# Performance work log

Hardware: AMD Instinct MI355X
Metric: run time of the kernel (lower is better)

The kernel has to match this reference:

```python
import jax, jax.numpy as jnp
import numpy as np

N = 50000
E = 600000
D = 128  # embedding_dimension


def _lrelu(x):
    return jax.nn.leaky_relu(x, negative_slope=0.01)


def _rgcn(x, edge_index, edge_type, rel_w, root_w, bias):
    # FastRGCNConv, num_relations=2, aggr='mean' (PyG default).
    # Compute per-relation transforms as 2 dense GEMMs, then gather per edge.
    h = jnp.einsum('nd,rde->rne', x, rel_w)          # [2, N, D]
    src, dst = edge_index[0], edge_index[1]
    msg = h[edge_type, src]                          # [E, D] gather
    agg = jax.ops.segment_sum(msg, dst, num_segments=x.shape[0])
    deg = jax.ops.segment_sum(jnp.ones((msg.shape[0],), x.dtype), dst,
                              num_segments=x.shape[0])
    agg = agg / jnp.maximum(deg, 1.0)[:, None]       # mean over in-edges
    return agg + x @ root_w + bias


def setup_inputs() -> dict:
    key = jax.random.key(0)
    ks = jax.random.split(key, 32)
    f32 = jnp.float32
    inp = {
        'des': jax.random.normal(ks[0], (N, 768), f32),
        'tweet': jax.random.normal(ks[1], (N, 768), f32),
        'num_prop': jax.random.normal(ks[2], (N, 7), f32),
        'cat_prop': jax.random.normal(ks[3], (N, 11), f32),
        'new_feature': jax.random.normal(ks[4], (N, 1), f32),
        'edge_index': jax.random.randint(ks[5], (2, E), 0, N),
        'edge_type': jax.random.randint(ks[6], (E,), 0, 2),
    }
    def lin(k, i, o, s=0.05):
        kw, kb = jax.random.split(k)
        return (jax.random.normal(kw, (i, o), f32) * s,
                jax.random.normal(kb, (o,), f32) * s)
    pf = D // 5  # 25
    inp['W_des'], inp['b_des'] = lin(ks[7], 768, pf)
    inp['W_tweet'], inp['b_tweet'] = lin(ks[8], 768, 28)
    inp['W_num'], inp['b_num'] = lin(ks[9], 7, pf)
    inp['W_cat'], inp['b_cat'] = lin(ks[10], 11, pf)
    inp['W_new'], inp['b_new'] = lin(ks[11], 1, pf)
    inp['W_in'], inp['b_in'] = lin(ks[12], D, D)
    inp['rel_w1'] = jax.random.normal(ks[13], (2, D, D), f32) * 0.05
    inp['root_w1'] = jax.random.normal(ks[14], (D, D), f32) * 0.05
    inp['bias1'] = jax.random.normal(ks[15], (D,), f32) * 0.05
    inp['rel_w2'] = jax.random.normal(ks[16], (2, D, D), f32) * 0.05
    inp['root_w2'] = jax.random.normal(ks[17], (D, D), f32) * 0.05
    inp['bias2'] = jax.random.normal(ks[18], (D,), f32) * 0.05
    inp['W_out1'], inp['b_out1'] = lin(ks[19], D, D)
    inp['W_out2'], inp['b_out2'] = lin(ks[20], D, 2)
    return inp


def reference(des, tweet, num_prop, cat_prop, new_feature,
              W_des, b_des, W_tweet, b_tweet, W_num, b_num,
              W_cat, b_cat, W_new, b_new, W_in, b_in,
              rel_w1, root_w1, bias1, rel_w2, root_w2, bias2,
              W_out1, b_out1, W_out2, b_out2,
              edge_index, edge_type):
    d = _lrelu(des @ W_des + b_des)
    t = _lrelu(tweet @ W_tweet + b_tweet)
    n = _lrelu(num_prop @ W_num + b_num)
    c = _lrelu(cat_prop @ W_cat + b_cat)
    nf = _lrelu(new_feature @ W_new + b_new)
    x = jnp.concatenate((d, t, n, c, nf), axis=1)  # [N, 128]
    x = _lrelu(x @ W_in + b_in)
    x = _rgcn(x, edge_index, edge_type, rel_w1, root_w1, bias1)
    # dropout is identity at eval time
    x = _rgcn(x, edge_index, edge_type, rel_w2, root_w2, bias2)
    x = _lrelu(x @ W_out1 + b_out1)
    return x @ W_out2 + b_out2  # [N, 2]
```

## Files before the change

### kernel.cpp

```cpp
#include <hip/hip_runtime.h>

#define N_NODES 50000
#define N_EDGES 600000
#define NPAD    50048
#define NBLK_SCAN 196

static __device__ __forceinline__ float lrelu(float v) {
    return v > 0.f ? v : 0.01f * v;
}

template<int NCOLS>
__device__ __forceinline__ void proj_body(
    const float* __restrict__ A, const float* __restrict__ W,
    float* __restrict__ P, int row, int kq)
{
    float acc[NCOLS];
    #pragma unroll
    for (int c = 0; c < NCOLS; c++) acc[c] = 0.f;

    const float4* Ar = (const float4*)(A + (size_t)row * 768 + kq * 192);
    const float*  Wp = W + (size_t)kq * 192 * NCOLS;

    #pragma unroll 8
    for (int j = 0; j < 48; j++) {
        float4 a = Ar[j];
        const float* w = Wp + j * 4 * NCOLS;
        #pragma unroll
        for (int c = 0; c < NCOLS; c++)
            acc[c] += a.x * w[c] + a.y * w[NCOLS + c]
                    + a.z * w[2 * NCOLS + c] + a.w * w[3 * NCOLS + c];
    }
    float* o = P + ((size_t)kq * N_NODES + row) * 32;
    #pragma unroll
    for (int c = 0; c < NCOLS; c++) o[c] = acc[c];
}

__global__ __launch_bounds__(256) void proj768_v4(
    const float* __restrict__ des, const float* __restrict__ Wd,
    const float* __restrict__ tw,  const float* __restrict__ Wt,
    float* __restrict__ P)
{
    const int row = blockIdx.x * 256 + threadIdx.x;
    if (row >= N_NODES) return;
    const int kq = blockIdx.y;
    if (blockIdx.z == 0) proj_body<25>(des, Wd, P, row, kq);
    else                 proj_body<28>(tw, Wt, P + (size_t)4 * N_NODES * 32, row, kq);
}

__global__ void combine_proj4(const float* __restrict__ P,
                              const float* __restrict__ bd, const float* __restrict__ bt,
                              float* __restrict__ X0)
{
    int id = blockIdx.x * 256 + threadIdx.x;
    int n = id >> 6, c = id & 63;
    if (n >= N_NODES || c >= 53) return;
    const float* base; int cc; float b;
    if (c < 25) { base = P;                              cc = c;      b = bd[cc]; }
    else        { base = P + (size_t)4 * N_NODES * 32;   cc = c - 25; b = bt[cc]; }
    float s = base[((size_t)0 * N_NODES + n) * 32 + cc]
            + base[((size_t)1 * N_NODES + n) * 32 + cc]
            + base[((size_t)2 * N_NODES + n) * 32 + cc]
            + base[((size_t)3 * N_NODES + n) * 32 + cc];
    X0[(size_t)n * 128 + c] = lrelu(s + b);
}

__global__ void small_proj_kernel(
    const float* __restrict__ nump, const float* __restrict__ catp, const float* __restrict__ newf,
    const float* __restrict__ Wn, const float* __restrict__ bn,
    const float* __restrict__ Wc, const float* __restrict__ bc,
    const float* __restrict__ Ww, const float* __restrict__ bw,
    float* __restrict__ out)
{
    int id = blockIdx.x * 256 + threadIdx.x;
    int n = id / 75, c = id % 75;
    if (n >= N_NODES) return;
    float acc; int col;
    if (c < 25) {
        col = 53 + c; acc = bn[c];
        #pragma unroll
        for (int k = 0; k < 7; k++) acc += nump[n * 7 + k] * Wn[k * 25 + c];
    } else if (c < 50) {
        int cc = c - 25; col = 78 + cc; acc = bc[cc];
        #pragma unroll
        for (int k = 0; k < 11; k++) acc += catp[n * 11 + k] * Wc[k * 25 + cc];
    } else {
        int cc = c - 50; col = 103 + cc;
        acc = bw[cc] + newf[n] * Ww[cc];
    }
    out[(size_t)n * 128 + col] = lrelu(acc);
}

template<int KTOT, bool SPLIT, bool ACT>
__global__ __launch_bounds__(256, 4) void gemm_v2(
    const float* __restrict__ A, const float* __restrict__ A2,
    const float* __restrict__ B, const float* __restrict__ B2,
    const float* __restrict__ bias, float* __restrict__ out)
{
    __shared__ float AlT[32 * 132];
    __shared__ float Bl [32 * 132];
    const int t  = threadIdx.x;
    const int r0 = blockIdx.x * 128;
    const int tx = t & 15, ty = t >> 4;

    float acc[8][8] = {};

    for (int k0 = 0; k0 < KTOT; k0 += 32) {
        #pragma unroll
        for (int i = 0; i < 4; i++) {
            int f4i = t + i * 256;
            int row = f4i >> 3, c4 = f4i & 7;
            int k = k0 + c4 * 4;
            float4 v;
            if (!SPLIT) {
                v = *(const float4*)&A[(size_t)(r0 + row) * 128 + k];
            } else {
                if (k < 256) v = *(const float4*)&A[(size_t)(r0 + row) * 256 + k];
                else         v = *(const float4*)&A2[(size_t)(r0 + row) * 128 + (k - 256)];
            }
            AlT[(c4 * 4 + 0) * 132 + row] = v.x;
            AlT[(c4 * 4 + 1) * 132 + row] = v.y;
            AlT[(c4 * 4 + 2) * 132 + row] = v.z;
            AlT[(c4 * 4 + 3) * 132 + row] = v.w;
        }
        #pragma unroll
        for (int i = 0; i < 4; i++) {
            int f4i = t + i * 256;
            int kk = f4i >> 5, c4 = f4i & 31;
            int k = k0 + kk;
            float4 v;
            if (!SPLIT) v = *(const float4*)&B[(size_t)k * 128 + c4 * 4];
            else v = (k < 256) ? *(const float4*)&B[(size_t)k * 128 + c4 * 4]
                               : *(const float4*)&B2[(size_t)(k - 256) * 128 + c4 * 4];
            *(float4*)&Bl[kk * 132 + c4 * 4] = v;
        }
        __syncthreads();
        #pragma unroll 4
        for (int k = 0; k < 32; k++) {
            float4 a0 = *(const float4*)&AlT[k * 132 + ty * 8];
            float4 a1 = *(const float4*)&AlT[k * 132 + ty * 8 + 4];
            float4 b0 = *(const float4*)&Bl [k * 132 + tx * 8];
            float4 b1 = *(const float4*)&Bl [k * 132 + tx * 8 + 4];
            float av[8] = {a0.x, a0.y, a0.z, a0.w, a1.x, a1.y, a1.z, a1.w};
            float bv[8] = {b0.x, b0.y, b0.z, b0.w, b1.x, b1.y, b1.z, b1.w};
            #pragma unroll
            for (int i = 0; i < 8; i++)
                #pragma unroll
                for (int j = 0; j < 8; j++) acc[i][j] += av[i] * bv[j];
        }
        __syncthreads();
    }
    float4 bb0 = *(const float4*)&bias[tx * 8];
    float4 bb1 = *(const float4*)&bias[tx * 8 + 4];
    float bb[8] = {bb0.x, bb0.y, bb0.z, bb0.w, bb1.x, bb1.y, bb1.z, bb1.w};
    #pragma unroll
    for (int i = 0; i < 8; i++) {
        size_t row = (size_t)(r0 + ty * 8 + i);
        float o[8];
        #pragma unroll
        for (int j = 0; j < 8; j++) {
            o[j] = acc[i][j] + bb[j];
            if (ACT) o[j] = lrelu(o[j]);
        }
        *(float4*)&out[row * 128 + tx * 8]     = make_float4(o[0], o[1], o[2], o[3]);
        *(float4*)&out[row * 128 + tx * 8 + 4] = make_float4(o[4], o[5], o[6], o[7]);
    }
}

__global__ void count_kernel(const int* __restrict__ ei, int* __restrict__ count) {
    int e = blockIdx.x * 256 + threadIdx.x;
    if (e < N_EDGES) atomicAdd(&count[ei[N_EDGES + e]], 1);
}

__global__ void scan1_kernel(const int* __restrict__ count, int* __restrict__ partial) {
    __shared__ int sm[256];
    int b = blockIdx.x, t = threadIdx.x;
    int i = b * 256 + t;
    sm[t] = (i < N_NODES) ? count[i] : 0;
    __syncthreads();
    for (int off = 128; off > 0; off >>= 1) {
        if (t < off) sm[t] += sm[t + off];
        __syncthreads();
    }
    if (t == 0) partial[b] = sm[0];
}

__global__ void scan2_kernel(int* __restrict__ partial) {
    __shared__ int sm[256];
    int t = threadIdx.x;
    int v = (t < NBLK_SCAN) ? partial[t] : 0;
    sm[t] = v; __syncthreads();
    for (int off = 1; off < 256; off <<= 1) {
        int add = (t >= off) ? sm[t - off] : 0;
        __syncthreads();
        sm[t] += add;
        __syncthreads();
    }
    partial[t] = sm[t] - v;
}

__global__ void scan3_kernel(const int* __restrict__ count, const int* __restrict__ partial,
                             int* __restrict__ offsets) {
    __shared__ int sm[256];
    int b = blockIdx.x, t = threadIdx.x;
    int i = b * 256 + t;
    int v = (i < N_NODES) ? count[i] : 0;
    sm[t] = v; __syncthreads();
    for (int off = 1; off < 256; off <<= 1) {
        int add = (t >= off) ? sm[t - off] : 0;
        __syncthreads();
        sm[t] += add;
        __syncthreads();
    }
    if (i < N_NODES) offsets[i] = partial[b] + sm[t] - v;
}

__global__ void fill_kernel(const int* __restrict__ ei, const int* __restrict__ et,
                            const int* __restrict__ offsets, int* __restrict__ cursor,
                            int* __restrict__ elist) {
    int e = blockIdx.x * 256 + threadIdx.x;
    if (e < N_EDGES) {
        int d = ei[N_EDGES + e];
        int pos = atomicAdd(&cursor[d], 1);
        elist[offsets[d] + pos] = (int)(((unsigned)ei[e]) | (((unsigned)et[e]) << 31));
    }
}

__global__ __launch_bounds__(256) void aggregate_v3(
    const float* __restrict__ x, const int* __restrict__ offsets,
    const int* __restrict__ count, const int* __restrict__ elist,
    float* __restrict__ s)
{
    int nid  = blockIdx.x * 8 + (threadIdx.x >> 5);
    int lane = threadIdx.x & 31;
    if (nid >= N_NODES) return;
    int start = offsets[nid], dg = count[nid];
    float4 a0 = make_float4(0.f, 0.f, 0.f, 0.f);
    float4 a1 = make_float4(0.f, 0.f, 0.f, 0.f);
    int i = 0;
    for (; i + 2 <= dg; i += 2) {
        int v0 = elist[start + i];
        int v1 = elist[start + i + 1];
        float4 u = ((const float4*)&x[(size_t)(v0 & 0x7FFFFFFF) * 128])[lane];
        float4 w = ((const float4*)&x[(size_t)(v1 & 0x7FFFFFFF) * 128])[lane];
        if (v0 < 0) { a1.x += u.x; a1.y += u.y; a1.z += u.z; a1.w += u.w; }
        else        { a0.x += u.x; a0.y += u.y; a0.z += u.z; a0.w += u.w; }
        if (v1 < 0) { a1.x += w.x; a1.y += w.y; a1.z += w.z; a1.w += w.w; }
        else        { a0.x += w.x; a0.y += w.y; a0.z += w.z; a0.w += w.w; }
    }
    if (i < dg) {
        int v0 = elist[start + i];
        float4 u = ((const float4*)&x[(size_t)(v0 & 0x7FFFFFFF) * 128])[lane];
        if (v0 < 0) { a1.x += u.x; a1.y += u.y; a1.z += u.z; a1.w += u.w; }
        else        { a0.x += u.x; a0.y += u.y; a0.z += u.z; a0.w += u.w; }
    }
    float inv = 1.0f / (float)(dg > 0 ? dg : 1);
    a0.x *= inv; a0.y *= inv; a0.z *= inv; a0.w *= inv;
    a1.x *= inv; a1.y *= inv; a1.z *= inv; a1.w *= inv;
    ((float4*)&s[(size_t)nid * 256])[lane]       = a0;
    ((float4*)&s[(size_t)nid * 256 + 128])[lane] = a1;
}

__global__ __launch_bounds__(64) void final_kernel(
    const float* __restrict__ x, const float* __restrict__ W2,
    const float* __restrict__ b2, float* __restrict__ out)
{
    int n = blockIdx.x;
    int t = threadIdx.x;
    float x0 = x[(size_t)n * 128 + t];
    float x1 = x[(size_t)n * 128 + 64 + t];
    float p0 = x0 * W2[t * 2]     + x1 * W2[(t + 64) * 2];
    float p1 = x0 * W2[t * 2 + 1] + x1 * W2[(t + 64) * 2 + 1];
    #pragma unroll
    for (int off = 32; off > 0; off >>= 1) {
        p0 += __shfl_down(p0, off);
        p1 += __shfl_down(p1, off);
    }
    if (t == 0) {
        out[(size_t)n * 2]     = p0 + b2[0];
        out[(size_t)n * 2 + 1] = p1 + b2[1];
    }
}

extern "C" void kernel_launch(void* const* d_in, const int* in_sizes, int n_in,
                              void* d_out, int out_size, void* d_ws, size_t ws_size,
                              hipStream_t stream)
{
    const float* des   = (const float*)d_in[0];
    const float* tw    = (const float*)d_in[1];
    const float* nump  = (const float*)d_in[2];
    const float* catp  = (const float*)d_in[3];
    const float* newf  = (const float*)d_in[4];
    const int*   ei    = (const int*)d_in[5];
    const int*   et    = (const int*)d_in[6];
    const float* Wd    = (const float*)d_in[7];  const float* bd  = (const float*)d_in[8];
    const float* Wt    = (const float*)d_in[9];  const float* bt  = (const float*)d_in[10];
    const float* Wn    = (const float*)d_in[11]; const float* bn  = (const float*)d_in[12];
    const float* Wc    = (const float*)d_in[13]; const float* bc  = (const float*)d_in[14];
    const float* Ww    = (const float*)d_in[15]; const float* bw  = (const float*)d_in[16];
    const float* Win   = (const float*)d_in[17]; const float* bin = (const float*)d_in[18];
    const float* relw1 = (const float*)d_in[19]; const float* rootw1 = (const float*)d_in[20];
    const float* bias1 = (const float*)d_in[21];
    const float* relw2 = (const float*)d_in[22]; const float* rootw2 = (const float*)d_in[23];
    const float* bias2 = (const float*)d_in[24];
    const float* Wo1   = (const float*)d_in[25]; const float* bo1 = (const float*)d_in[26];
    const float* Wo2   = (const float*)d_in[27]; const float* bo2 = (const float*)d_in[28];
    float* outp = (float*)d_out;

    char* ws = (char*)d_ws;
    const size_t szX = (size_t)NPAD * 128 * sizeof(float);
    float* X0 = (float*)(ws);
    float* X1 = (float*)(ws + szX);
    float* S  = (float*)(ws + 2 * szX);
    float* P  = S;
    char* p = ws + 2 * szX + (size_t)NPAD * 256 * sizeof(float);
    int* count   = (int*)p; p += (size_t)NPAD * 4;
    int* offsets = (int*)p; p += (size_t)NPAD * 4;
    int* cursor  = (int*)p; p += (size_t)NPAD * 4;
    int* elist   = (int*)p; p += (size_t)N_EDGES * 4;
    int* partial = (int*)p;

    hipMemsetAsync(count,  0, NPAD * sizeof(int), stream);
    hipMemsetAsync(cursor, 0, NPAD * sizeof(int), stream);

    dim3 pg((N_NODES + 255) / 256, 4, 2);
    proj768_v4<<<pg, 256, 0, stream>>>(des, Wd, tw, Wt, P);
    small_proj_kernel<<<(N_NODES * 75 + 255) / 256, 256, 0, stream>>>(
        nump, catp, newf, Wn, bn, Wc, bc, Ww, bw, X0);
    combine_proj4<<<(N_NODES * 64 + 255) / 256, 256, 0, stream>>>(P, bd, bt, X0);
    gemm_v2<128, false, true><<<NPAD / 128, 256, 0, stream>>>(
        X0, nullptr, Win, nullptr, bin, X1);

    count_kernel<<<(N_EDGES + 255) / 256, 256, 0, stream>>>(ei, count);
    scan1_kernel<<<NBLK_SCAN, 256, 0, stream>>>(count, partial);
    scan2_kernel<<<1, 256, 0, stream>>>(partial);
    scan3_kernel<<<NBLK_SCAN, 256, 0, stream>>>(count, partial, offsets);
    fill_kernel<<<(N_EDGES + 255) / 256, 256, 0, stream>>>(ei, et, offsets, cursor, elist);

    aggregate_v3<<<(N_NODES + 7) / 8, 256, 0, stream>>>(X1, offsets, count, elist, S);
    gemm_v2<384, true, false><<<NPAD / 128, 256, 0, stream>>>(
        S, X1, relw1, rootw1, bias1, X0);

    aggregate_v3<<<(N_NODES + 7) / 8, 256, 0, stream>>>(X0, offsets, count, elist, S);
    gemm_v2<384, true, false><<<NPAD / 128, 256, 0, stream>>>(
        S, X0, relw2, rootw2, bias2, X1);

    gemm_v2<128, false, true><<<NPAD / 128, 256, 0, stream>>>(
        X1, nullptr, Wo1, nullptr, bo1, X0);
    final_kernel<<<N_NODES, 64, 0, stream>>>(X0, Wo2, bo2, outp);
}
```

Measured before the change: 870.6 us.

## Stage 768-wide projection rows through LDS and fuse bias/activation epilogue

```diff
diff --git a/kernel.cpp b/kernel.cpp
--- a/kernel.cpp
+++ b/kernel.cpp
@@ -9,59 +9,68 @@
     return v > 0.f ? v : 0.01f * v;
 }
 
-template<int NCOLS>
-__device__ __forceinline__ void proj_body(
+#define RS_P 129
+
+template<int NC>
+__device__ __forceinline__ void proj_lds_body(
     const float* __restrict__ A, const float* __restrict__ W,
-    float* __restrict__ P, int row, int kq)
-{
-    float acc[NCOLS];
+    const float* __restrict__ bias, float* __restrict__ X0,
+    int colbase, float* AlT)
+{
+    constexpr int CH = (NC + 1) / 2;
+    const int t    = threadIdx.x;
+    const int row  = t & 127;
+    const int half = t >> 7;
+    const int c0   = __builtin_amdgcn_readfirstlane(half ? (NC - CH) : 0);
+    const int r0   = blockIdx.x * 128;
+    const int q    = t & 7;
+
+    float acc[CH];
     #pragma unroll
-    for (int c = 0; c < NCOLS; c++) acc[c] = 0.f;
-
-    const float4* Ar = (const float4*)(A + (size_t)row * 768 + kq * 192);
-    const float*  Wp = W + (size_t)kq * 192 * NCOLS;
-
-    #pragma unroll 8
-    for (int j = 0; j < 48; j++) {
-        float4 a = Ar[j];
-        const float* w = Wp + j * 4 * NCOLS;
-        #pragma unroll
-        for (int c = 0; c < NCOLS; c++)
-            acc[c] += a.x * w[c] + a.y * w[NCOLS + c]
-                    + a.z * w[2 * NCOLS + c] + a.w * w[3 * NCOLS + c];
-    }
-    float* o = P + ((size_t)kq * N_NODES + row) * 32;
-    #pragma unroll
-    for (int c = 0; c < NCOLS; c++) o[c] = acc[c];
-}
-
-__global__ __launch_bounds__(256) void proj768_v4(
-    const float* __restrict__ des, const float* __restrict__ Wd,
-    const float* __restrict__ tw,  const float* __restrict__ Wt,
-    float* __restrict__ P)
-{
-    const int row = blockIdx.x * 256 + threadIdx.x;
-    if (row >= N_NODES) return;
-    const int kq = blockIdx.y;
-    if (blockIdx.z == 0) proj_body<25>(des, Wd, P, row, kq);
-    else                 proj_body<28>(tw, Wt, P + (size_t)4 * N_NODES * 32, row, kq);
-}
-
-__global__ void combine_proj4(const float* __restrict__ P,
-                              const float* __restrict__ bd, const float* __restrict__ bt,
-                              float* __restrict__ X0)
-{
-    int id = blockIdx.x * 256 + threadIdx.x;
-    int n = id >> 6, c = id & 63;
-    if (n >= N_NODES || c >= 53) return;
-    const float* base; int cc; float b;
-    if (c < 25) { base = P;                              cc = c;      b = bd[cc]; }
-    else        { base = P + (size_t)4 * N_NODES * 32;   cc = c - 25; b = bt[cc]; }
-    float s = base[((size_t)0 * N_NODES + n) * 32 + cc]
-            + base[((size_t)1 * N_NODES + n) * 32 + cc]
-            + base[((size_t)2 * N_NODES + n) * 32 + cc]
-            + base[((size_t)3 * N_NODES + n) * 32 + cc];
-    X0[(size_t)n * 128 + c] = lrelu(s + b);
+    for (int c = 0; c < CH; c++) acc[c] = 0.f;
+
+    for (int k0 = 0; k0 < 768; k0 += 32) {
+        __syncthreads();
+        #pragma unroll
+        for (int i = 0; i < 4; i++) {
+            int rr = i * 32 + (t >> 3);
+            int gr = r0 + rr;
+            float4 v = make_float4(0.f, 0.f, 0.f, 0.f);
+            if (gr < N_NODES)
+                v = *(const float4*)&A[(size_t)gr * 768 + k0 + q * 4];
+            AlT[(q * 4 + 0) * RS_P + rr] = v.x;
+            AlT[(q * 4 + 1) * RS_P + rr] = v.y;
+            AlT[(q * 4 + 2) * RS_P + rr] = v.z;
+            AlT[(q * 4 + 3) * RS_P + rr] = v.w;
+        }
+        __syncthreads();
+        const float* Wk = W + (size_t)k0 * NC + c0;
+        #pragma unroll
+        for (int k = 0; k < 32; k++) {
+            float a = AlT[k * RS_P + row];
+            const float* w = Wk + k * NC;
+            #pragma unroll
+            for (int c = 0; c < CH; c++) acc[c] += a * w[c];
+        }
+    }
+    int grow = r0 + row;
+    if (grow < N_NODES) {
+        #pragma unroll
+        for (int c = 0; c < CH; c++) {
+            float v = lrelu(acc[c] + bias[c0 + c]);
+            X0[(size_t)grow * 128 + colbase + c0 + c] = v;
+        }
+    }
+}
+
+__global__ __launch_bounds__(256) void proj768_lds(
+    const float* __restrict__ des, const float* __restrict__ Wd, const float* __restrict__ bd,
+    const float* __restrict__ tw,  const float* __restrict__ Wt, const float* __restrict__ bt,
+    float* __restrict__ X0)
+{
+    __shared__ float AlT[32 * RS_P];
+    if (blockIdx.z == 0) proj_lds_body<25>(des, Wd, bd, X0, 0,  AlT);
+    else                 proj_lds_body<28>(tw, Wt, bt, X0, 25, AlT);
 }
 
 __global__ void small_proj_kernel(
@@ -311,7 +320,6 @@
     float* X0 = (float*)(ws);
     float* X1 = (float*)(ws + szX);
     float* S  = (float*)(ws + 2 * szX);
-    float* P  = S;
     char* p = ws + 2 * szX + (size_t)NPAD * 256 * sizeof(float);
     int* count   = (int*)p; p += (size_t)NPAD * 4;
     int* offsets = (int*)p; p += (size_t)NPAD * 4;
@@ -322,11 +330,10 @@
     hipMemsetAsync(count,  0, NPAD * sizeof(int), stream);
     hipMemsetAsync(cursor, 0, NPAD * sizeof(int), stream);
 
-    dim3 pg((N_NODES + 255) / 256, 4, 2);
-    proj768_v4<<<pg, 256, 0, stream>>>(des, Wd, tw, Wt, P);
+    dim3 pg(NPAD / 128, 1, 2);
+    proj768_lds<<<pg, 256, 0, stream>>>(des, Wd, bd, tw, Wt, bt, X0);
     small_proj_kernel<<<(N_NODES * 75 + 255) / 256, 256, 0, stream>>>(
         nump, catp, newf, Wn, bn, Wc, bc, Ww, bw, X0);
-    combine_proj4<<<(N_NODES * 64 + 255) / 256, 256, 0, stream>>>(P, bd, bt, X0);
     gemm_v2<128, false, true><<<NPAD / 128, 256, 0, stream>>>(
         X0, nullptr, Win, nullptr, bin, X1);
 
```

After: 953.8 us. +9.6%, slower.

## Stream 768-wide projections with coalesced row reads and fused bias/activation

Applied to the files above, without the earlier changes.

```diff
diff --git a/kernel.cpp b/kernel.cpp
--- a/kernel.cpp
+++ b/kernel.cpp
@@ -9,59 +9,80 @@
     return v > 0.f ? v : 0.01f * v;
 }
 
-template<int NCOLS>
-__device__ __forceinline__ void proj_body(
-    const float* __restrict__ A, const float* __restrict__ W,
-    float* __restrict__ P, int row, int kq)
-{
-    float acc[NCOLS];
+#define WP_DES_F4   (192 * 25)
+#define WP_TW_F4    (192 * 28)
+__global__ void pack_w_kernel(const float* __restrict__ Wd, const float* __restrict__ Wt,
+                              float* __restrict__ Wp)
+{
+    int id = blockIdx.x * 256 + threadIdx.x;
+    int total = (WP_DES_F4 + WP_TW_F4) * 4;
+    if (id >= total) return;
+    float v;
+    if (id < WP_DES_F4 * 4) {
+        int f4 = id >> 2, j = id & 3;
+        int k4 = f4 / 25, c = f4 % 25;
+        v = Wd[(k4 * 4 + j) * 25 + c];
+    } else {
+        int id2 = id - WP_DES_F4 * 4;
+        int f4 = id2 >> 2, j = id2 & 3;
+        int k4 = f4 / 28, c = f4 % 28;
+        v = Wt[(k4 * 4 + j) * 28 + c];
+    }
+    Wp[id] = v;
+}
+
+template<int NC>
+__device__ __forceinline__ void proj_stream_body(
+    const float* __restrict__ A, const float4* __restrict__ Wp,
+    const float* __restrict__ bias, float* __restrict__ X0, int colbase)
+{
+    const int l    = threadIdx.x & 63;
+    const int wv   = threadIdx.x >> 6;
+    const int q    = l & 7;
+    const int rsub = l >> 3;
+    const int row  = blockIdx.x * 32 + wv * 8 + rsub;
+    const int rcl  = row < N_NODES ? row : N_NODES - 1;
+    const float4* Ar = (const float4*)(A + (size_t)rcl * 768);
+
+    float acc[NC];
     #pragma unroll
-    for (int c = 0; c < NCOLS; c++) acc[c] = 0.f;
-
-    const float4* Ar = (const float4*)(A + (size_t)row * 768 + kq * 192);
-    const float*  Wp = W + (size_t)kq * 192 * NCOLS;
-
-    #pragma unroll 8
-    for (int j = 0; j < 48; j++) {
-        float4 a = Ar[j];
-        const float* w = Wp + j * 4 * NCOLS;
-        #pragma unroll
-        for (int c = 0; c < NCOLS; c++)
-            acc[c] += a.x * w[c] + a.y * w[NCOLS + c]
-                    + a.z * w[2 * NCOLS + c] + a.w * w[3 * NCOLS + c];
-    }
-    float* o = P + ((size_t)kq * N_NODES + row) * 32;
+    for (int c = 0; c < NC; c++) acc[c] = 0.f;
+
+    #pragma unroll 2
+    for (int it = 0; it < 24; it++) {
+        float4 a = Ar[it * 8 + q];
+        const float4* wp = Wp + (it * 8 + q) * NC;
+        #pragma unroll
+        for (int c = 0; c < NC; c++) {
+            float4 w = wp[c];
+            acc[c] += a.x * w.x + a.y * w.y + a.z * w.z + a.w * w.w;
+        }
+    }
+
     #pragma unroll
-    for (int c = 0; c < NCOLS; c++) o[c] = acc[c];
-}
-
-__global__ __launch_bounds__(256) void proj768_v4(
-    const float* __restrict__ des, const float* __restrict__ Wd,
-    const float* __restrict__ tw,  const float* __restrict__ Wt,
-    float* __restrict__ P)
-{
-    const int row = blockIdx.x * 256 + threadIdx.x;
-    if (row >= N_NODES) return;
-    const int kq = blockIdx.y;
-    if (blockIdx.z == 0) proj_body<25>(des, Wd, P, row, kq);
-    else                 proj_body<28>(tw, Wt, P + (size_t)4 * N_NODES * 32, row, kq);
-}
-
-__global__ void combine_proj4(const float* __restrict__ P,
-                              const float* __restrict__ bd, const float* __restrict__ bt,
-                              float* __restrict__ X0)
-{
-    int id = blockIdx.x * 256 + threadIdx.x;
-    int n = id >> 6, c = id & 63;
-    if (n >= N_NODES || c >= 53) return;
-    const float* base; int cc; float b;
-    if (c < 25) { base = P;                              cc = c;      b = bd[cc]; }
-    else        { base = P + (size_t)4 * N_NODES * 32;   cc = c - 25; b = bt[cc]; }
-    float s = base[((size_t)0 * N_NODES + n) * 32 + cc]
-            + base[((size_t)1 * N_NODES + n) * 32 + cc]
-            + base[((size_t)2 * N_NODES + n) * 32 + cc]
-            + base[((size_t)3 * N_NODES + n) * 32 + cc];
-    X0[(size_t)n * 128 + c] = lrelu(s + b);
+    for (int c = 0; c < NC; c++) {
+        float v = acc[c];
+        v += __shfl_xor(v, 1);
+        v += __shfl_xor(v, 2);
+        v += __shfl_xor(v, 4);
+        acc[c] = v;
+    }
+    if (q == 0 && row < N_NODES) {
+        #pragma unroll
+        for (int c = 0; c < NC; c++)
+            X0[(size_t)row * 128 + colbase + c] = lrelu(acc[c] + bias[c]);
+    }
+}
+
+__global__ __launch_bounds__(256) void proj_stream(
+    const float* __restrict__ des, const float* __restrict__ tw,
+    const float* __restrict__ Wp, const float* __restrict__ bd,
+    const float* __restrict__ bt, float* __restrict__ X0)
+{
+    if (blockIdx.z == 0)
+        proj_stream_body<25>(des, (const float4*)Wp, bd, X0, 0);
+    else
+        proj_stream_body<28>(tw, (const float4*)Wp + WP_DES_F4, bt, X0, 25);
 }
 
 __global__ void small_proj_kernel(
@@ -311,7 +332,7 @@
     float* X0 = (float*)(ws);
     float* X1 = (float*)(ws + szX);
     float* S  = (float*)(ws + 2 * szX);
-    float* P  = S;
+    float* Wp = S;
     char* p = ws + 2 * szX + (size_t)NPAD * 256 * sizeof(float);
     int* count   = (int*)p; p += (size_t)NPAD * 4;
     int* offsets = (int*)p; p += (size_t)NPAD * 4;
@@ -322,11 +343,11 @@
     hipMemsetAsync(count,  0, NPAD * sizeof(int), stream);
     hipMemsetAsync(cursor, 0, NPAD * sizeof(int), stream);
 
-    dim3 pg((N_NODES + 255) / 256, 4, 2);
-    proj768_v4<<<pg, 256, 0, stream>>>(des, Wd, tw, Wt, P);
+    pack_w_kernel<<<((WP_DES_F4 + WP_TW_F4) * 4 + 255) / 256, 256, 0, stream>>>(Wd, Wt, Wp);
+    dim3 pg((N_NODES + 31) / 32, 1, 2);
+    proj_stream<<<pg, 256, 0, stream>>>(des, tw, Wp, bd, bt, X0);
     small_proj_kernel<<<(N_NODES * 75 + 255) / 256, 256, 0, stream>>>(
         nump, catp, newf, Wn, bn, Wc, bc, Ww, bw, X0);
-    combine_proj4<<<(N_NODES * 64 + 255) / 256, 256, 0, stream>>>(P, bd, bt, X0);
     gemm_v2<128, false, true><<<NPAD / 128, 256, 0, stream>>>(
         X0, nullptr, Win, nullptr, bin, X1);
 
```

Result: slower. 1.261 ms (+44.8%).
